# Kernel optimization log

Measured on AMD Instinct MI355X. Metric: run time of the kernel, lower is better.

The kernel has to match this reference:

```python
import jax, jax.numpy as jnp
import numpy as np

# ---- dims (match init_kwargs) ----
B0, C0, H0, W0 = 16, 64, 128, 128
G = 8            # d_model of inner Mamba2
D_STATE = 16
D_CONV = 3
EXPAND = 2
HEADDIM = 8
D_INNER = EXPAND * G            # 16
NHEADS = D_INNER // HEADDIM     # 2
NGROUPS = 1
CONV_DIM = D_INNER + 2 * NGROUPS * D_STATE   # 48
D_IN_PROJ = 2 * D_INNER + 2 * NGROUPS * D_STATE + NHEADS  # 66
EPS = 1e-5


def silu(x):
    return x * jax.nn.sigmoid(x)


def setup_inputs() -> dict:
    key = jax.random.key(0)
    ks = jax.random.split(key, 12)
    s = 0.02
    return {
        "x": jax.random.normal(ks[0], (B0, C0, H0, W0), jnp.float32),
        # 1x1 conv tokenize / detokenize (stored as matrices)
        "w_tok": jax.random.normal(ks[1], (G, C0), jnp.float32) * s,
        "b_tok": jnp.zeros((G,), jnp.float32),
        "w_detok": jax.random.normal(ks[2], (C0, G), jnp.float32) * s,
        "b_detok": jnp.zeros((C0,), jnp.float32),
        # Mamba2 params
        "w_in": jax.random.normal(ks[3], (D_IN_PROJ, G), jnp.float32) * s,
        "w_conv": jax.random.normal(ks[4], (CONV_DIM, 1, D_CONV), jnp.float32) * s,
        "b_conv": jnp.zeros((CONV_DIM,), jnp.float32),
        "dt_bias": jax.random.uniform(ks[5], (NHEADS,), jnp.float32, -4.0, -2.0),
        "A_log": jnp.log(jnp.arange(1, NHEADS + 1, dtype=jnp.float32)),
        "D": jnp.ones((NHEADS,), jnp.float32),
        "norm_w": jnp.ones((D_INNER,), jnp.float32),
        "w_out": jax.random.normal(ks[6], (G, D_INNER), jnp.float32) * s,
    }


def _mamba2(u, w_in, w_conv, b_conv, dt_bias, A_log, D, norm_w, w_out):
    # u: [B, L, G]
    Bb, L, _ = u.shape
    zxbcdt = jnp.einsum('blg,dg->bld', u, w_in)                 # [B,L,66]
    z = zxbcdt[..., :D_INNER]                                   # [B,L,16]
    xBC = zxbcdt[..., D_INNER:D_INNER + CONV_DIM]               # [B,L,48]
    dt = jax.nn.softplus(zxbcdt[..., D_INNER + CONV_DIM:] + dt_bias)  # [B,L,H]

    # causal depthwise conv1d over time
    xBC_t = jnp.moveaxis(xBC, 1, 2)                             # [B,48,L]
    xBC_t = jnp.pad(xBC_t, ((0, 0), (0, 0), (D_CONV - 1, 0)))
    xBC_t = jax.lax.conv_general_dilated(
        xBC_t, w_conv, window_strides=(1,), padding='VALID',
        dimension_numbers=('NCH', 'OIH', 'NCH'), feature_group_count=CONV_DIM)
    xBC = silu(jnp.moveaxis(xBC_t + b_conv[None, :, None], 1, 2))  # [B,L,48]

    xh = xBC[..., :D_INNER].reshape(Bb, L, NHEADS, HEADDIM)     # [B,L,H,P]
    Bm = xBC[..., D_INNER:D_INNER + D_STATE]                    # [B,L,N] (ngroups=1)
    Cm = xBC[..., D_INNER + D_STATE:]                           # [B,L,N]

    A = -jnp.exp(A_log)                                         # [H]
    dA = jnp.exp(dt * A)                                        # [B,L,H]

    # time-major sequential selective scan
    def step(state, inp):
        dA_t, dt_t, x_t, B_t, C_t = inp  # [B,H],[B,H],[B,H,P],[B,N],[B,N]
        state = state * dA_t[:, :, None, None] \
            + (dt_t[:, :, None] * x_t)[..., None] * B_t[:, None, None, :]
        y = jnp.einsum('bhpn,bn->bhp', state, C_t)
        return state, y

    init = jnp.zeros((Bb, NHEADS, HEADDIM, D_STATE), u.dtype)
    xs = (jnp.moveaxis(dA, 1, 0), jnp.moveaxis(dt, 1, 0),
          jnp.moveaxis(xh, 1, 0), jnp.moveaxis(Bm, 1, 0), jnp.moveaxis(Cm, 1, 0))
    _, ys = jax.lax.scan(step, init, xs)                        # [L,B,H,P]
    y = jnp.moveaxis(ys, 0, 1) + D[None, None, :, None] * xh    # [B,L,H,P]
    y = y.reshape(Bb, L, D_INNER)

    # gated RMSNorm then out projection
    y = y * silu(z)
    y = y * jax.lax.rsqrt(jnp.mean(y * y, axis=-1, keepdims=True) + EPS) * norm_w
    return jnp.einsum('bld,gd->blg', y, w_out)


def reference(x, w_tok, b_tok, w_detok, b_detok, w_in, w_conv, b_conv,
              dt_bias, A_log, D, norm_w, w_out):
    Bb, C, H, W = x.shape
    g = jnp.einsum('bchw,gc->bghw', x, w_tok) + b_tok[None, :, None, None]
    g = g.reshape(Bb, G, H * W).transpose(0, 2, 1)              # [B,HW,G]
    g = _mamba2(g, w_in, w_conv, b_conv, dt_bias, A_log, D, norm_w, w_out) + g
    g = g.transpose(0, 2, 1).reshape(Bb, G, H, W)
    return x + jnp.einsum('bghw,cg->bchw', g, w_detok) + b_detok[None, :, None, None]
```

## Files before the change

kernel.cpp:

```cpp
#include <hip/hip_runtime.h>

namespace {
constexpr int NB   = 16;
constexpr int NC   = 64;
constexpr int HW   = 128*128;
constexpr int SL   = 16384;
constexpr int CQ   = 64;
constexpr int NCH  = SL/CQ;
constexpr int PWV  = 9728;

typedef short short8 __attribute__((ext_vector_type(8)));
typedef float f32x4  __attribute__((ext_vector_type(4)));

__device__ __forceinline__ float frcp(float x){ return __builtin_amdgcn_rcpf(x); }
__device__ __forceinline__ float rl(float v, int s){
  return __int_as_float(__builtin_amdgcn_readlane(__float_as_int(v), s));
}
__device__ __forceinline__ float sigu(float a){ return frcp(1.0f + __expf(-a)); }
__device__ __forceinline__ float softplusf(float a){
  return fmaxf(a, 0.f) + __logf(1.f + __expf(-fabsf(a)));
}
__device__ __forceinline__ unsigned bfr(float x){
  unsigned u = __float_as_uint(x);
  u = u + 0x7FFF + ((u>>16)&1);
  return u>>16;
}
__device__ __forceinline__ unsigned pk2(float a, float b){
  return (bfr(a)&0xFFFFu) | (bfr(b)<<16);
}
__device__ __forceinline__ float blo(unsigned u){ return __uint_as_float(u<<16); }
__device__ __forceinline__ float bhi(unsigned u){ return __uint_as_float(u & 0xFFFF0000u); }
union CV8 { unsigned u[4]; short8 s; };

__global__ __launch_bounds__(256) void k_tok(
    const float* __restrict__ x, const float* __restrict__ w_tok,
    const float* __restrict__ b_tok, float* __restrict__ g0,
    const float* __restrict__ w_in, const float* __restrict__ w_conv,
    unsigned short* __restrict__ weff)
{
  if (blockIdx.x == 0) {
    for (int i = threadIdx.x; i < 64*32; i += 256) {
      int j = i >> 5, k = i & 31;
      float v = 0.f;
      if (j < 48) {
        if (k < 24) v = w_conv[j*3 + (k>>3)] * w_in[(16+j)*8 + (k&7)];
      } else if (j < 50) {
        if (k >= 16 && k < 24) v = w_in[(64 + (j-48))*8 + (k-16)];
      }
      weff[i] = (unsigned short)bfr(v);
    }
  }
  __shared__ float s_wt[NC][8];
  __shared__ float s_bt[8];
  for (int i = threadIdx.x; i < NC*8; i += 256) s_wt[i>>3][i&7] = w_tok[(i&7)*NC + (i>>3)];
  if (threadIdx.x < 8) s_bt[threadIdx.x] = b_tok[threadIdx.x];
  __syncthreads();
  long idx = (long)blockIdx.x * 256 + threadIdx.x;
  int b = (int)(idx >> 14);
  int l = (int)(idx & (SL-1));
  float acc[8];
  #pragma unroll
  for (int g = 0; g < 8; ++g) acc[g] = s_bt[g];
  const float* xp = x + (long)b*NC*HW + l;
  #pragma unroll 8
  for (int c = 0; c < NC; ++c) {
    float v = xp[(long)c*HW];
    const float4* wr = (const float4*)s_wt[c];
    float4 w0 = wr[0], w1 = wr[1];
    acc[0] += v*w0.x; acc[1] += v*w0.y; acc[2] += v*w0.z; acc[3] += v*w0.w;
    acc[4] += v*w1.x; acc[5] += v*w1.y; acc[6] += v*w1.z; acc[7] += v*w1.w;
  }
  float* gp = g0 + idx*8;
  *(float4*)gp     = make_float4(acc[0],acc[1],acc[2],acc[3]);
  *(float4*)(gp+4) = make_float4(acc[4],acc[5],acc[6],acc[7]);
}

__global__ __launch_bounds__(256) void k_front(
    const float* __restrict__ g0, const unsigned short* __restrict__ weff,
    const float* __restrict__ b_conv,
    const float* __restrict__ dt_bias, const float* __restrict__ A_log,
    const float* __restrict__ Dvec,
    float* __restrict__ Sc, float* __restrict__ Pc,
    float* __restrict__ ceg, unsigned short* __restrict__ Cg,
    float* __restrict__ Yg)
{
  __shared__ float s_bc[48];
  __shared__ float s_misc[8];
  __shared__ char  s_wv[4][PWV];

  int tid = threadIdx.x, lane = tid & 63, wave = tid >> 6;
  int c15 = lane & 15, lg = lane >> 4;

  if (tid < 48) s_bc[tid] = b_conv[tid];
  if (tid < 2) {
    s_misc[tid]   = -__expf(A_log[tid]);
    s_misc[2+tid] = dt_bias[tid];
    s_misc[4+tid] = Dvec[tid];
  }
  __syncthreads();

  int b   = blockIdx.x >> 6;
  int chB = (blockIdx.x & 63)*4 + wave;
  long cg = (long)b*NCH + chB;
  int l0  = chB*CQ;
  char* WR = s_wv[wave];
  char* BT  = WR;
  char* uB  = WR + 2048;
  char* uC  = WR + 4096;
  char* Xp  = WR + 6144;
  char* Mb  = WR;
  char* ytr = WR;
  char* dtL = WR + 8192;
  char* cfL = WR + 8704;
  char* ceL = WR + 9216;

  short8 zero8 = {0,0,0,0,0,0,0,0};
  f32x4  zero4 = {0.f,0.f,0.f,0.f};

  short8 Af[4];
  #pragma unroll
  for (int tt = 0; tt < 4; ++tt) {
    int p = l0 + 16*tt + c15 - 2 + lg;
    bool ok = (lg < 3) && (p >= 0);
    const float* up = g0 + ((long)b*SL + (ok ? p : 0))*8;
    float4 a = *(const float4*)up, c = *(const float4*)(up+4);
    CV8 w;
    w.u[0] = pk2(a.x,a.y); w.u[1] = pk2(a.z,a.w);
    w.u[2] = pk2(c.x,c.y); w.u[3] = pk2(c.z,c.w);
    Af[tt] = ok ? w.s : zero8;
  }

  f32x4 xg[4];
  #pragma unroll
  for (int jj = 0; jj < 4; ++jj) {
    short8 Wf = *(const short8*)(weff + (16*jj + c15)*32 + lg*8);
    f32x4 o[4];
    #pragma unroll
    for (int tt = 0; tt < 4; ++tt)
      o[tt] = __builtin_amdgcn_mfma_f32_16x16x32_bf16(Af[tt], Wf, zero4, 0,0,0);
    if (jj == 3) {
      if (c15 < 2) {
        float bias = s_misc[2+c15];
        #pragma unroll
        for (int tt = 0; tt < 4; ++tt) {
          #pragma unroll
          for (int r = 0; r < 4; ++r)
            *(float*)(dtL + c15*256 + (16*tt + 4*lg + r)*4) = o[tt][r] + bias;
        }
      }
    } else {
      float bias = s_bc[16*jj + c15];
      #pragma unroll
      for (int tt = 0; tt < 4; ++tt) {
        float s0 = (o[tt][0]+bias), s1 = (o[tt][1]+bias);
        float s2 = (o[tt][2]+bias), s3 = (o[tt][3]+bias);
        s0 *= sigu(s0); s1 *= sigu(s1); s2 *= sigu(s2); s3 *= sigu(s3);
        int t0 = 16*tt + 4*lg;
        if (jj == 0) {
          f32x4 v; v[0]=s0; v[1]=s1; v[2]=s2; v[3]=s3;
          xg[tt] = v;
        } else if (jj == 1) {
          uint2 wv; wv.x = pk2(s0,s1); wv.y = pk2(s2,s3);
          *(uint2*)(BT + c15*128 + ((t0*2) ^ ((c15&7)<<4))) = wv;
          *(short*)(uB + (t0  )*32 + c15*2) = (short)bfr(s0);
          *(short*)(uB + (t0+1)*32 + c15*2) = (short)bfr(s1);
          *(short*)(uB + (t0+2)*32 + c15*2) = (short)bfr(s2);
          *(short*)(uB + (t0+3)*32 + c15*2) = (short)bfr(s3);
        } else {
          *(short*)(uC + (t0  )*32 + c15*2) = (short)bfr(s0);
          *(short*)(uC + (t0+1)*32 + c15*2) = (short)bfr(s1);
          *(short*)(uC + (t0+2)*32 + c15*2) = (short)bfr(s2);
          *(short*)(uC + (t0+3)*32 + c15*2) = (short)bfr(s3);
        }
      }
    }
  }
  __builtin_amdgcn_wave_barrier();
  __builtin_amdgcn_sched_barrier(0x7F);

  float dt0 = softplusf(*(const float*)(dtL + lane*4));
  float dt1 = softplusf(*(const float*)(dtL + 256 + lane*4));
  float c0 = s_misc[0]*dt0, c1 = s_misc[1]*dt1;
  #pragma unroll
  for (int off = 1; off < 64; off <<= 1) {
    float t0 = __shfl_up(c0, off), t1 = __shfl_up(c1, off);
    if (lane >= off) { c0 += t0; c1 += t1; }
  }
  float ce0 = __expf(c0), ce1 = __expf(c1);
  float cf0 = __expf(-c0)*dt0, cf1 = __expf(-c1)*dt1;
  float cee0 = rl(ce0, 63), cee1 = rl(ce1, 63);
  ceg[cg*128 + lane]      = ce0;
  ceg[cg*128 + 64 + lane] = ce1;
  if (lane == 0) { Pc[cg*2] = cee0; Pc[cg*2+1] = cee1; }
  *(float*)(cfL + lane*4)       = cf0;
  *(float*)(cfL + 256 + lane*4) = cf1;
  *(float*)(ceL + lane*4)       = ce0;
  *(float*)(ceL + 256 + lane*4) = ce1;
  __builtin_amdgcn_wave_barrier();
  __builtin_amdgcn_sched_barrier(0x7F);

  int hh = (c15 < 8) ? 0 : 1;
  #pragma unroll
  for (int tt = 0; tt < 4; ++tt) {
    int t0 = 16*tt + 4*lg;
    float4 cf4 = *(const float4*)(cfL + hh*256 + t0*4);
    uint2 wv;
    wv.x = pk2(cf4.x*xg[tt][0], cf4.y*xg[tt][1]);
    wv.y = pk2(cf4.z*xg[tt][2], cf4.w*xg[tt][3]);
    *(uint2*)(Xp + c15*128 + ((t0*2) ^ ((c15&7)<<4))) = wv;
  }
  __builtin_amdgcn_wave_barrier();
  __builtin_amdgcn_sched_barrier(0x7F);

  { short8 ca = *(const short8*)(uC + lane*32);
    short8 cb = *(const short8*)(uC + lane*32 + 16);
    *(short8*)(Cg + cg*1024 + lane*16)     = ca;
    *(short8*)(Cg + cg*1024 + lane*16 + 8) = cb; }

  { f32x4 sacc = zero4;
    #pragma unroll
    for (int kb = 0; kb < 2; ++kb) {
      int cb2 = (64*kb + 16*lg) ^ ((c15&7)<<4);
      short8 Afx = *(const short8*)(Xp + c15*128 + cb2);
      short8 Bfx = *(const short8*)(BT + c15*128 + cb2);
      sacc = __builtin_amdgcn_mfma_f32_16x16x32_bf16(Afx, Bfx, sacc, 0,0,0);
    }
    float cee = (lg < 2) ? cee0 : cee1;
    #pragma unroll
    for (int r = 0; r < 4; ++r)
      Sc[cg*256 + (4*lg+r)*16 + c15] = cee*sacc[r];
  }

  short8 Cfr[4], Bfr[4], Xf[2];
  #pragma unroll
  for (int tt = 0; tt < 4; ++tt) {
    Cfr[tt] = zero8; Bfr[tt] = zero8;
    if (lg < 2) {
      Cfr[tt] = *(const short8*)(uC + (16*tt + c15)*32 + 16*lg);
      Bfr[tt] = *(const short8*)(uB + (16*tt + c15)*32 + 16*lg);
    }
  }
  #pragma unroll
  for (int kb = 0; kb < 2; ++kb)
    Xf[kb] = *(const short8*)(Xp + c15*128 + ((64*kb + 16*lg) ^ ((c15&7)<<4)));
  __builtin_amdgcn_wave_barrier();
  __builtin_amdgcn_sched_barrier(0x7F);

  #pragma unroll
  for (int tt = 0; tt < 4; ++tt) {
    int t  = 16*tt + c15;
    int sw = (t&7)<<4;
    #pragma unroll
    for (int ts = 0; ts < 4; ++ts) {
      if (ts <= tt) {
        f32x4 gA = __builtin_amdgcn_mfma_f32_16x16x32_bf16(Bfr[ts], Cfr[tt], zero4, 0,0,0);
        if (ts == tt) {
          #pragma unroll
          for (int r = 0; r < 4; ++r)
            gA[r] = (4*lg + r <= c15) ? gA[r] : 0.f;
        }
        uint2 wv; wv.x = pk2(gA[0],gA[1]); wv.y = pk2(gA[2],gA[3]);
        *(uint2*)(Mb + t*128 + ((32*ts + 8*lg) ^ sw)) = wv;
      }
    }
    if (tt == 0 || tt == 2) {
      uint2 zv; zv.x = 0u; zv.y = 0u;
      *(uint2*)(Mb + t*128 + ((32*(tt+1) + 8*lg) ^ sw)) = zv;
    }
  }
  __builtin_amdgcn_wave_barrier();
  __builtin_amdgcn_sched_barrier(0x7F);

  f32x4 acc[4];
  #pragma unroll
  for (int tt = 0; tt < 4; ++tt) acc[tt] = zero4;
  #pragma unroll
  for (int tt = 0; tt < 4; ++tt) {
    int t = 16*tt + c15, sw = (t&7)<<4;
    { short8 Mf = *(const short8*)(Mb + t*128 + ((16*lg) ^ sw));
      acc[tt] = __builtin_amdgcn_mfma_f32_16x16x32_bf16(Mf, Xf[0], acc[tt], 0,0,0); }
    if (tt >= 2) {
      short8 Mf = *(const short8*)(Mb + t*128 + ((64 + 16*lg) ^ sw));
      acc[tt] = __builtin_amdgcn_mfma_f32_16x16x32_bf16(Mf, Xf[1], acc[tt], 0,0,0);
    }
  }
  __builtin_amdgcn_sched_barrier(0x7F);

  float Dh = (c15 < 8) ? s_misc[4] : s_misc[5];
  #pragma unroll
  for (int tt = 0; tt < 4; ++tt) {
    int t0 = 16*tt + 4*lg;
    float4 ce4 = *(const float4*)(ceL + hh*256 + t0*4);
    *(float*)(ytr + (t0  )*96 + c15*4) = ce4.x*acc[tt][0] + Dh*xg[tt][0];
    *(float*)(ytr + (t0+1)*96 + c15*4) = ce4.y*acc[tt][1] + Dh*xg[tt][1];
    *(float*)(ytr + (t0+2)*96 + c15*4) = ce4.z*acc[tt][2] + Dh*xg[tt][2];
    *(float*)(ytr + (t0+3)*96 + c15*4) = ce4.w*acc[tt][3] + Dh*xg[tt][3];
  }
  __builtin_amdgcn_wave_barrier();
  __builtin_amdgcn_sched_barrier(0x7F);

  float* yg = Yg + cg*1024 + lane*16;
  #pragma unroll
  for (int i = 0; i < 4; ++i) {
    float4 q = *(const float4*)(ytr + lane*96 + i*16);
    *(float4*)(yg + 4*i) = q;
  }
}

__global__ __launch_bounds__(256) void k_scan(
    const float* __restrict__ Sc, const float* __restrict__ Pc,
    float* __restrict__ Stin)
{
  int b = blockIdx.x;
  int tid = threadIdx.x;
  int h = tid >> 7;
  float st = 0.f;
  long base = (long)b * NCH;
  #pragma unroll 8
  for (int c = 0; c < NCH; ++c) {
    Stin[(base + c)*256 + tid] = st;
    st = st * Pc[(base + c)*2 + h] + Sc[(base + c)*256 + tid];
  }
}

__global__ __launch_bounds__(256) void k_out(
    const float* __restrict__ g0, const float* __restrict__ w_in,
    const float* __restrict__ norm_w, const float* __restrict__ w_out,
    const float* __restrict__ Stin, const float* __restrict__ ceg,
    const unsigned short* __restrict__ Cg, const float* __restrict__ Yg,
    const float* __restrict__ x, const float* __restrict__ w_detok,
    const float* __restrict__ b_detok, float* __restrict__ out)
{
  __shared__ float s_win[16][8];
  __shared__ float s_wout[8][16];
  __shared__ float s_nw[16];
  __shared__ float s_st[4][256];
  __shared__ float s_og[8][256];

  int tid = threadIdx.x, lane = tid & 63, wave = tid >> 6;
  int b   = blockIdx.x >> 6;

  int c  = tid >> 2;
  int qq = tid & 3;
  int l0b = (blockIdx.x & 63) * 256;
  const float* xp = x + (long)b*NC*HW + (long)c*HW + l0b;
  float4 xpre[8];
  #pragma unroll
  for (int k = 0; k < 8; ++k) xpre[k] = *(const float4*)(xp + (qq + 4*k)*4);

  if (tid < 128) s_win[tid>>3][tid&7] = w_in[tid];
  if (tid < 128) s_wout[tid>>4][tid&15] = w_out[tid];
  if (tid < 16)  s_nw[tid] = norm_w[tid];
  __syncthreads();

  auto dot8 = [&](const float* uu, int row) -> float {
    const float4* wr = (const float4*)s_win[row];
    float4 w0 = wr[0], w1 = wr[1];
    return uu[0]*w0.x + uu[1]*w0.y + uu[2]*w0.z + uu[3]*w0.w
         + uu[4]*w1.x + uu[5]*w1.y + uu[6]*w1.z + uu[7]*w1.w;
  };

  int chB = (blockIdx.x & 63)*4 + wave;
  long cg = (long)b*NCH + chB;
  long pos = (long)b*SL + chB*CQ + lane;

  { float4 t4 = *(const float4*)(Stin + cg*256 + lane*4);
    *(float4*)&s_st[wave][lane*4] = t4; }

  float u[8];
  { const float* up = g0 + pos*8;
    float4 a = *(const float4*)up, c2 = *(const float4*)(up+4);
    u[0]=a.x;u[1]=a.y;u[2]=a.z;u[3]=a.w;u[4]=c2.x;u[5]=c2.y;u[6]=c2.z;u[7]=c2.w; }

  float Cr[16];
  { const uint4* cp = (const uint4*)(Cg + cg*1024 + lane*16);
    uint4 ca = cp[0], cb = cp[1];
    Cr[0]=blo(ca.x); Cr[1]=bhi(ca.x); Cr[2]=blo(ca.y); Cr[3]=bhi(ca.y);
    Cr[4]=blo(ca.z); Cr[5]=bhi(ca.z); Cr[6]=blo(ca.w); Cr[7]=bhi(ca.w);
    Cr[8]=blo(cb.x); Cr[9]=bhi(cb.x); Cr[10]=blo(cb.y); Cr[11]=bhi(cb.y);
    Cr[12]=blo(cb.z); Cr[13]=bhi(cb.z); Cr[14]=blo(cb.w); Cr[15]=bhi(cb.w); }

  float yr[16];
  { const float* yp = Yg + cg*1024 + lane*16;
    #pragma unroll
    for (int i = 0; i < 4; ++i) {
      float4 q = *(const float4*)(yp + 4*i);
      yr[4*i]=q.x; yr[4*i+1]=q.y; yr[4*i+2]=q.z; yr[4*i+3]=q.w;
    } }
  float ce0t = ceg[cg*128 + lane];
  float ce1t = ceg[cg*128 + 64 + lane];

  __builtin_amdgcn_wave_barrier();
  __builtin_amdgcn_sched_barrier(0x7F);

  const float* st = &s_st[wave][0];
  float y[16];
  #pragma unroll
  for (int hp = 0; hp < 16; ++hp) {
    const float4* sp = (const float4*)(st + hp*16);
    float4 s0 = sp[0], s1 = sp[1], s2 = sp[2], s3 = sp[3];
    float a = Cr[0]*s0.x + Cr[1]*s0.y + Cr[2]*s0.z + Cr[3]*s0.w
            + Cr[4]*s1.x + Cr[5]*s1.y + Cr[6]*s1.z + Cr[7]*s1.w
            + Cr[8]*s2.x + Cr[9]*s2.y + Cr[10]*s2.z + Cr[11]*s2.w
            + Cr[12]*s3.x + Cr[13]*s3.y + Cr[14]*s3.z + Cr[15]*s3.w;
    y[hp] = yr[hp] + ((hp < 8) ? ce0t : ce1t)*a;
  }

  float yv[16]; float ss = 0.f;
  #pragma unroll
  for (int d = 0; d < 16; ++d) {
    float zz = dot8(u, d);
    float v = y[d] * (zz * sigu(zz));
    yv[d] = v; ss += v*v;
  }
  float scn = rsqrtf(ss*(1.f/16.f) + 1e-5f);
  { const float4* nw = (const float4*)s_nw;
    float4 n0 = nw[0], n1 = nw[1], n2 = nw[2], n3 = nw[3];
    yv[0]*=scn*n0.x; yv[1]*=scn*n0.y; yv[2]*=scn*n0.z; yv[3]*=scn*n0.w;
    yv[4]*=scn*n1.x; yv[5]*=scn*n1.y; yv[6]*=scn*n1.z; yv[7]*=scn*n1.w;
    yv[8]*=scn*n2.x; yv[9]*=scn*n2.y; yv[10]*=scn*n2.z; yv[11]*=scn*n2.w;
    yv[12]*=scn*n3.x; yv[13]*=scn*n3.y; yv[14]*=scn*n3.z; yv[15]*=scn*n3.w; }
  int posL = wave*64 + lane;
  #pragma unroll
  for (int g = 0; g < 8; ++g) {
    const float4* wr = (const float4*)s_wout[g];
    float4 w0 = wr[0], w1 = wr[1], w2 = wr[2], w3 = wr[3];
    float a = u[g];
    a += yv[0]*w0.x + yv[1]*w0.y + yv[2]*w0.z + yv[3]*w0.w;
    a += yv[4]*w1.x + yv[5]*w1.y + yv[6]*w1.z + yv[7]*w1.w;
    a += yv[8]*w2.x + yv[9]*w2.y + yv[10]*w2.z + yv[11]*w2.w;
    a += yv[12]*w3.x + yv[13]*w3.y + yv[14]*w3.z + yv[15]*w3.w;
    s_og[g][posL] = a;
  }
  __syncthreads();

  float* op = out + (long)b*NC*HW + (long)c*HW + l0b;
  float wd[8];
  { float4 wa = *(const float4*)(w_detok + c*8);
    float4 wb = *(const float4*)(w_detok + c*8 + 4);
    wd[0]=wa.x; wd[1]=wa.y; wd[2]=wa.z; wd[3]=wa.w;
    wd[4]=wb.x; wd[5]=wb.y; wd[6]=wb.z; wd[7]=wb.w; }
  float bd = b_detok[c];

  #pragma unroll 4
  for (int k = 0; k < 16; ++k) {
    int q = qq + 4*k;
    float4 xv = (k < 8) ? xpre[k] : *(const float4*)(xp + q*4);
    float r0 = xv.x + bd, r1 = xv.y + bd, r2 = xv.z + bd, r3 = xv.w + bd;
    #pragma unroll
    for (int g = 0; g < 8; ++g) {
      float4 o4 = *(const float4*)&s_og[g][q*4];
      r0 += o4.x*wd[g]; r1 += o4.y*wd[g];
      r2 += o4.z*wd[g]; r3 += o4.w*wd[g];
    }
    *(float4*)(op + q*4) = make_float4(r0,r1,r2,r3);
  }
}
}

extern "C" void kernel_launch(void* const* d_in, const int* in_sizes, int n_in,
                              void* d_out, int out_size, void* d_ws, size_t ws_size,
                              hipStream_t stream)
{
  const float* x       = (const float*)d_in[0];
  const float* w_tok   = (const float*)d_in[1];
  const float* b_tok   = (const float*)d_in[2];
  const float* w_detok = (const float*)d_in[3];
  const float* b_detok = (const float*)d_in[4];
  const float* w_in    = (const float*)d_in[5];
  const float* w_conv  = (const float*)d_in[6];
  const float* b_conv  = (const float*)d_in[7];
  const float* dt_bias = (const float*)d_in[8];
  const float* A_log   = (const float*)d_in[9];
  const float* Dvec    = (const float*)d_in[10];
  const float* norm_w  = (const float*)d_in[11];
  const float* w_out   = (const float*)d_in[12];
  float* out = (float*)d_out;

  float* ws   = (float*)d_ws;
  float* g0   = ws;
  float* Sc   = g0 + (long)NB*SL*8;
  float* Pc   = Sc + (long)NB*NCH*256;
  float* Stin = Pc + (long)NB*NCH*2;
  float* ceg  = Stin + (long)NB*NCH*256;
  float* Yg   = ceg + (long)NB*NCH*128;
  unsigned short* Cg = (unsigned short*)(Yg + (long)NB*NCH*1024);
  unsigned short* weff = Cg + (long)NB*NCH*1024;

  k_tok<<<NB*SL/256, 256, 0, stream>>>(x, w_tok, b_tok, g0, w_in, w_conv, weff);
  k_front<<<NB*NCH/4, 256, 0, stream>>>(g0, weff, b_conv, dt_bias,
                                        A_log, Dvec, Sc, Pc, ceg, Cg, Yg);
  k_scan<<<NB, 256, 0, stream>>>(Sc, Pc, Stin);
  k_out<<<NB*NCH/4, 256, 0, stream>>>(g0, w_in, norm_w, w_out,
                                      Stin, ceg, Cg, Yg,
                                      x, w_detok, b_detok, out);
}
```

Before: 112.0 us.

## Restructure k_out into single-wave blocks with wave-level sync only

k_out now launches one 64-thread block per 64-token chunk instead of four chunks per 256-thread block. Each lane handles one output channel across 64 positions, which lets the block-wide __syncthreads calls be replaced by wave barriers. The early prefetch of x before the weight staging is dropped. The per-channel access pattern means each lane reads and writes 64 contiguous floats from a different channel row, so global accesses are strided across lanes (4 KB-aligned, 256 B segments per lane) instead of coalesced. Small weight staging is also repeated in four times as many blocks.

```diff
diff --git a/kernel.cpp b/kernel.cpp
--- a/kernel.cpp
+++ b/kernel.cpp
@@ -323,7 +323,7 @@
   }
 }
 
-__global__ __launch_bounds__(256) void k_out(
+__global__ __launch_bounds__(64) void k_out(
     const float* __restrict__ g0, const float* __restrict__ w_in,
     const float* __restrict__ norm_w, const float* __restrict__ w_out,
     const float* __restrict__ Stin, const float* __restrict__ ceg,
@@ -334,38 +334,21 @@
   __shared__ float s_win[16][8];
   __shared__ float s_wout[8][16];
   __shared__ float s_nw[16];
-  __shared__ float s_st[4][256];
-  __shared__ float s_og[8][256];
-
-  int tid = threadIdx.x, lane = tid & 63, wave = tid >> 6;
-  int b   = blockIdx.x >> 6;
-
-  int c  = tid >> 2;
-  int qq = tid & 3;
-  int l0b = (blockIdx.x & 63) * 256;
-  const float* xp = x + (long)b*NC*HW + (long)c*HW + l0b;
-  float4 xpre[8];
-  #pragma unroll
-  for (int k = 0; k < 8; ++k) xpre[k] = *(const float4*)(xp + (qq + 4*k)*4);
-
-  if (tid < 128) s_win[tid>>3][tid&7] = w_in[tid];
-  if (tid < 128) s_wout[tid>>4][tid&15] = w_out[tid];
-  if (tid < 16)  s_nw[tid] = norm_w[tid];
-  __syncthreads();
-
-  auto dot8 = [&](const float* uu, int row) -> float {
-    const float4* wr = (const float4*)s_win[row];
-    float4 w0 = wr[0], w1 = wr[1];
-    return uu[0]*w0.x + uu[1]*w0.y + uu[2]*w0.z + uu[3]*w0.w
-         + uu[4]*w1.x + uu[5]*w1.y + uu[6]*w1.z + uu[7]*w1.w;
-  };
-
-  int chB = (blockIdx.x & 63)*4 + wave;
+  __shared__ float s_st[256];
+  __shared__ float s_og[8][64];
+
+  int lane = threadIdx.x;
+  int b   = blockIdx.x >> 8;
+  int chB = blockIdx.x & 255;
   long cg = (long)b*NCH + chB;
   long pos = (long)b*SL + chB*CQ + lane;
 
+  for (int i = lane; i < 128; i += 64) s_win[i>>3][i&7] = w_in[i];
+  for (int i = lane; i < 128; i += 64) s_wout[i>>4][i&15] = w_out[i];
+  if (lane < 16) s_nw[lane] = norm_w[lane];
+
   { float4 t4 = *(const float4*)(Stin + cg*256 + lane*4);
-    *(float4*)&s_st[wave][lane*4] = t4; }
+    *(float4*)&s_st[lane*4] = t4; }
 
   float u[8];
   { const float* up = g0 + pos*8;
@@ -393,11 +376,10 @@
   __builtin_amdgcn_wave_barrier();
   __builtin_amdgcn_sched_barrier(0x7F);
 
-  const float* st = &s_st[wave][0];
   float y[16];
   #pragma unroll
   for (int hp = 0; hp < 16; ++hp) {
-    const float4* sp = (const float4*)(st + hp*16);
+    const float4* sp = (const float4*)(&s_st[hp*16]);
     float4 s0 = sp[0], s1 = sp[1], s2 = sp[2], s3 = sp[3];
     float a = Cr[0]*s0.x + Cr[1]*s0.y + Cr[2]*s0.z + Cr[3]*s0.w
             + Cr[4]*s1.x + Cr[5]*s1.y + Cr[6]*s1.z + Cr[7]*s1.w
@@ -405,6 +387,13 @@
             + Cr[12]*s3.x + Cr[13]*s3.y + Cr[14]*s3.z + Cr[15]*s3.w;
     y[hp] = yr[hp] + ((hp < 8) ? ce0t : ce1t)*a;
   }
+
+  auto dot8 = [&](const float* uu, int row) -> float {
+    const float4* wr = (const float4*)s_win[row];
+    float4 w0 = wr[0], w1 = wr[1];
+    return uu[0]*w0.x + uu[1]*w0.y + uu[2]*w0.z + uu[3]*w0.w
+         + uu[4]*w1.x + uu[5]*w1.y + uu[6]*w1.z + uu[7]*w1.w;
+  };
 
   float yv[16]; float ss = 0.f;
   #pragma unroll
@@ -420,7 +409,6 @@
     yv[4]*=scn*n1.x; yv[5]*=scn*n1.y; yv[6]*=scn*n1.z; yv[7]*=scn*n1.w;
     yv[8]*=scn*n2.x; yv[9]*=scn*n2.y; yv[10]*=scn*n2.z; yv[11]*=scn*n2.w;
     yv[12]*=scn*n3.x; yv[13]*=scn*n3.y; yv[14]*=scn*n3.z; yv[15]*=scn*n3.w; }
-  int posL = wave*64 + lane;
   #pragma unroll
   for (int g = 0; g < 8; ++g) {
     const float4* wr = (const float4*)s_wout[g];
@@ -430,11 +418,15 @@
     a += yv[4]*w1.x + yv[5]*w1.y + yv[6]*w1.z + yv[7]*w1.w;
     a += yv[8]*w2.x + yv[9]*w2.y + yv[10]*w2.z + yv[11]*w2.w;
     a += yv[12]*w3.x + yv[13]*w3.y + yv[14]*w3.z + yv[15]*w3.w;
-    s_og[g][posL] = a;
-  }
-  __syncthreads();
-
-  float* op = out + (long)b*NC*HW + (long)c*HW + l0b;
+    s_og[g][lane] = a;
+  }
+  __builtin_amdgcn_wave_barrier();
+  __builtin_amdgcn_sched_barrier(0x7F);
+
+  int c = lane;
+  int l0c = chB*CQ;
+  const float* xp = x + (long)b*NC*HW + (long)c*HW + l0c;
+  float* op = out + (long)b*NC*HW + (long)c*HW + l0c;
   float wd[8];
   { float4 wa = *(const float4*)(w_detok + c*8);
     float4 wb = *(const float4*)(w_detok + c*8 + 4);
@@ -444,16 +436,15 @@
 
   #pragma unroll 4
   for (int k = 0; k < 16; ++k) {
-    int q = qq + 4*k;
-    float4 xv = (k < 8) ? xpre[k] : *(const float4*)(xp + q*4);
+    float4 xv = *(const float4*)(xp + k*4);
     float r0 = xv.x + bd, r1 = xv.y + bd, r2 = xv.z + bd, r3 = xv.w + bd;
     #pragma unroll
     for (int g = 0; g < 8; ++g) {
-      float4 o4 = *(const float4*)&s_og[g][q*4];
+      float4 o4 = *(const float4*)&s_og[g][k*4];
       r0 += o4.x*wd[g]; r1 += o4.y*wd[g];
       r2 += o4.z*wd[g]; r3 += o4.w*wd[g];
     }
-    *(float4*)(op + q*4) = make_float4(r0,r1,r2,r3);
+    *(float4*)(op + k*4) = make_float4(r0,r1,r2,r3);
   }
 }
 }
@@ -491,7 +482,7 @@
   k_front<<<NB*NCH/4, 256, 0, stream>>>(g0, weff, b_conv, dt_bias,
                                         A_log, Dvec, Sc, Pc, ceg, Cg, Yg);
   k_scan<<<NB, 256, 0, stream>>>(Sc, Pc, Stin);
-  k_out<<<NB*NCH/4, 256, 0, stream>>>(g0, w_in, norm_w, w_out,
-                                      Stin, ceg, Cg, Yg,
-                                      x, w_detok, b_detok, out);
-}
+  k_out<<<NB*NCH, 64, 0, stream>>>(g0, w_in, norm_w, w_out,
+                                   Stin, ceg, Cg, Yg,
+                                   x, w_detok, b_detok, out);
+}
```

Result: slower. 151.5 us (+35.2%).
